# Kernel optimization log

Measured on AMD Instinct MI355X. Metric: run time of the kernel, lower is better.

## Reference

```python
import jax, jax.numpy as jnp
import numpy as np
from jax import lax

DIM = 1024
HEADS = 16
KERNEL = 7
STRIDE = 4
EPS = 1e-5


def setup_inputs() -> dict:
    key = jax.random.key(0)
    ks = jax.random.split(key, 4)
    B, N = 2, 4096
    w_scale = 0.02
    return {
        "x": jax.random.normal(ks[0], (B, N, DIM), dtype=jnp.float32),
        "ln_w": jnp.ones((DIM,), jnp.float32),
        "ln_b": jnp.zeros((DIM,), jnp.float32),
        "Wk": jax.random.normal(ks[1], (DIM, DIM, KERNEL), dtype=jnp.float32) * w_scale,
        "Wv": jax.random.normal(ks[2], (DIM, DIM, KERNEL), dtype=jnp.float32) * w_scale,
        "Wq": jax.random.normal(ks[3], (DIM, DIM, KERNEL), dtype=jnp.float32) * w_scale,
    }


def _conv1d(x_bnd, w):
    # x: (B, N, D) -> conv over sequence dim with 'same' padding; w: (out_ch, in_ch, K)
    x_cn = jnp.transpose(x_bnd, (0, 2, 1))  # (B, D, N)
    pad = KERNEL // 2
    y = lax.conv_general_dilated(
        x_cn, w, window_strides=(1,), padding=[(pad, pad)],
        dimension_numbers=("NCH", "OIH", "NCH"))
    return jnp.transpose(y, (0, 2, 1))  # (B, N, D)


def reference(x, ln_w, ln_b, Wk, Wv, Wq):
    B, N, D = x.shape
    hd = D // HEADS
    # LayerNorm (biased variance, as in torch)
    mu = jnp.mean(x, axis=-1, keepdims=True)
    var = jnp.mean(jnp.square(x - mu), axis=-1, keepdims=True)
    x_n = (x - mu) / jnp.sqrt(var + EPS) * ln_w + ln_b

    K = _conv1d(x_n, Wk)                 # (B, N, D)
    V = _conv1d(x_n, Wv)                 # (B, N, D)
    Q = _conv1d(x_n, Wq)[:, ::STRIDE]    # (B, M, D) windowed queries
    M = Q.shape[1]

    Qh = Q.reshape(B, M, HEADS, hd).transpose(0, 2, 1, 3)  # (B, H, M, hd)
    Kh = K.reshape(B, N, HEADS, hd).transpose(0, 2, 1, 3)  # (B, H, N, hd)
    Vh = V.reshape(B, N, HEADS, hd).transpose(0, 2, 1, 3)  # (B, H, N, hd)

    scale = jnp.sqrt(jnp.asarray(hd, x.dtype))
    scores = jnp.einsum("bhmd,bhnd->bhmn", Qh, Kh) / scale  # (B, H, M, N)
    attn = jax.nn.softmax(scores, axis=-1)
    out = jnp.einsum("bhmn,bhnd->bhmd", attn, Vh)           # (B, H, M, hd)
    out = out.transpose(0, 2, 1, 3).reshape(B, M, D)
    return out + Q
```

## Files before the change

kernel.cpp:

```cpp
#include <hip/hip_runtime.h>

typedef __attribute__((ext_vector_type(4))) float f32x4;
typedef __attribute__((ext_vector_type(16))) float f32x16;
typedef __attribute__((ext_vector_type(8))) short short8;
typedef __attribute__((ext_vector_type(4))) unsigned short u16x4;
typedef __attribute__((ext_vector_type(8))) unsigned short u16x8;

#define AS1 __attribute__((address_space(1)))
#define AS3 __attribute__((address_space(3)))

__device__ __forceinline__ unsigned short f2bf(float f) {
  unsigned u = __float_as_uint(f);
  return (unsigned short)((u + 0x7FFFu + ((u >> 16) & 1u)) >> 16);
}
__device__ __forceinline__ unsigned short f2bf_fast(float f) {
  return (unsigned short)((__float_as_uint(f) + 0x8000u) >> 16);
}

__global__ __launch_bounds__(256) void ln_kernel(
    const float* __restrict__ x, const float* __restrict__ lw,
    const float* __restrict__ lb, unsigned short* __restrict__ xpad) {
  __shared__ float red[8];
  int row = blockIdx.x;
  int b = row >> 12, n = row & 4095;
  const float* xr = x + (size_t)row * 1024;
  int c = threadIdx.x * 4;
  f32x4 v = *(const f32x4*)(xr + c);
  float s = v[0] + v[1] + v[2] + v[3];
  float sq = v[0]*v[0] + v[1]*v[1] + v[2]*v[2] + v[3]*v[3];
#pragma unroll
  for (int off = 32; off; off >>= 1) {
    s  += __shfl_xor(s, off, 64);
    sq += __shfl_xor(sq, off, 64);
  }
  int w = threadIdx.x >> 6;
  if ((threadIdx.x & 63) == 0) { red[w*2] = s; red[w*2+1] = sq; }
  __syncthreads();
  float S  = red[0]+red[2]+red[4]+red[6];
  float SQ = red[1]+red[3]+red[5]+red[7];
  float mean = S * (1.0f/1024.0f);
  float var  = SQ * (1.0f/1024.0f) - mean*mean;
  float rstd = rsqrtf(var + 1e-5f);
  f32x4 wv = *(const f32x4*)(lw + c);
  f32x4 bv = *(const f32x4*)(lb + c);
  u16x4 o;
#pragma unroll
  for (int r = 0; r < 4; ++r) o[r] = f2bf((v[r]-mean)*rstd*wv[r] + bv[r]);
  *(u16x4*)(xpad + (((size_t)(b*4102 + n + 3)) << 10) + c) = o;
}

__global__ __launch_bounds__(256) void repack_kernel(
    const float* __restrict__ Wk, const float* __restrict__ Wv,
    const float* __restrict__ Wq, unsigned short* __restrict__ Wt) {
  __shared__ unsigned short t[7168];
  const float* W = (blockIdx.y == 0) ? Wk : (blockIdx.y == 1) ? Wv : Wq;
  int o = blockIdx.x;
  const float* row = W + (size_t)o * 7168;
  unsigned short* orow = Wt + ((size_t)(blockIdx.y * 1024 + o)) * 7168;
#pragma unroll
  for (int p = 0; p < 7; ++p) {
    int idx = p*1024 + threadIdx.x*4;
    f32x4 v = *(const f32x4*)(row + idx);
#pragma unroll
    for (int e = 0; e < 4; ++e) {
      unsigned j = idx + e;
      unsigned i = (j * 149797u) >> 20;
      unsigned k = j - i*7;
      t[k*1024 + i] = f2bf(v[e]);
    }
  }
  __syncthreads();
#pragma unroll
  for (int p = 0; p < 7; ++p) {
    int idx = p*1024 + threadIdx.x*4;
    *(u16x4*)(orow + idx) = *(const u16x4*)(t + idx);
  }
}

__global__ __launch_bounds__(256, 4) void conv3(
    const unsigned short* __restrict__ Apad,
    const unsigned short* __restrict__ Wt,
    unsigned short* __restrict__ Ksg, unsigned short* __restrict__ Vsg,
    unsigned short* __restrict__ Qsg, float* __restrict__ Qf) {
  __shared__ unsigned short As[128*64];
  __shared__ unsigned short Bs[128*64];
  const int g = blockIdx.x;
  const int tid = threadIdx.x;
  const int w = tid >> 6, l = tid & 63;

  int mode, nt, rt;
  if (g < 1024) {
    int xcol = ((g & 7) << 1) | ((g >> 3) & 1);
    mode = (xcol < 8) ? 0 : 1;
    nt = xcol; rt = g >> 4;
  } else {
    int gq = g - 1024;
    mode = 2; nt = 16 + (gq & 7); rt = gq >> 3;
  }
  const int n0 = nt << 7;
  const int r0 = rt << 7;

  const int lrow = l >> 3;
  const int cs = (l & 7) ^ lrow;
  size_t abase0, astep, bbase0;
  {
    int r = r0 + (w << 5) + lrow;
    int bb, nn;
    if (mode == 2) { bb = r >> 10; nn = (r & 1023) << 2; astep = 8 * 4096; }
    else           { bb = r >> 12; nn = r & 4095;        astep = 8 * 1024; }
    abase0 = (((size_t)(bb*4102 + nn)) << 10) + cs*8;
    int nc = n0 + (w << 5) + lrow;
    bbase0 = (size_t)nc * 7168 + cs*8;
  }

  f32x16 acc[2][2] = {};
  const int wm = (w >> 1) << 6, wn = (w & 1) << 6;
  const int l31 = l & 31, lh = l >> 5, l7 = l & 7;

  for (int k0 = 0; k0 < 7168; k0 += 64) {
    __syncthreads();
#pragma unroll
    for (int t = 0; t < 4; ++t) {
      __builtin_amdgcn_global_load_lds((const AS1 void*)(Apad + abase0 + (size_t)t*astep + k0),
                                       (AS3 void*)(As + (((w << 2) + t) << 9)), 16, 0, 0);
      __builtin_amdgcn_global_load_lds((const AS1 void*)(Wt + bbase0 + (size_t)t*(8*7168) + k0),
                                       (AS3 void*)(Bs + (((w << 2) + t) << 9)), 16, 0, 0);
    }
    __syncthreads();
#pragma unroll
    for (int s2 = 0; s2 < 2; ++s2) {
      short8 af[2][2], bf[2][2];
#pragma unroll
      for (int i = 0; i < 2; ++i)
#pragma unroll
        for (int hs = 0; hs < 2; ++hs) {
          int s = (s2 << 1) | hs;
          int ch = (((s << 1) | lh) ^ l7) << 3;
          af[i][hs] = *(const short8*)(As + (wm + (i<<5) + l31)*64 + ch);
          bf[i][hs] = *(const short8*)(Bs + (wn + (i<<5) + l31)*64 + ch);
        }
#pragma unroll
      for (int hs = 0; hs < 2; ++hs)
#pragma unroll
        for (int i = 0; i < 2; ++i)
#pragma unroll
          for (int j = 0; j < 2; ++j)
            acc[i][j] = __builtin_amdgcn_mfma_f32_32x32x16_bf16(af[i][hs], bf[j][hs], acc[i][j], 0, 0, 0);
    }
  }

  if (mode == 0) {
#pragma unroll
    for (int i = 0; i < 2; ++i) {
      int rgb = r0 + wm + (i<<5);
      int b = rgb >> 12, nbase = rgb & 4095;
#pragma unroll
      for (int j = 0; j < 2; ++j) {
        int cg = n0 + wn + (j<<5) + l31;
        int h = cg >> 6, kd = (cg >> 5) & 1;
        size_t base = ((size_t)(((b*16 + h)*2 + kd)) << 12) * 32 + (size_t)(cg & 31);
#pragma unroll
        for (int r = 0; r < 16; ++r) {
          int nb = nbase + (r & 3) + ((r >> 2) << 3) + (lh << 2);
          Ksg[base + ((size_t)nb << 5)] = f2bf(acc[i][j][r]);
        }
      }
    }
  } else if (mode == 1) {
#pragma unroll
    for (int i = 0; i < 2; ++i) {
      int rgb = r0 + wm + (i<<5);
      int b = rgb >> 12, nbase = rgb & 4095;
      int nc = nbase >> 5;
#pragma unroll
      for (int j = 0; j < 2; ++j) {
        int c = n0 + wn + (j<<5) + l31 - 1024;
        int h = c >> 6, d = c & 63;
        size_t rowbase = ((size_t)((b*16 + h)*128 + nc) * 64 + d) << 5;
#pragma unroll
        for (int g2 = 0; g2 < 4; ++g2) {
          u16x4 pv;
#pragma unroll
          for (int e = 0; e < 4; ++e) pv[e] = f2bf(acc[i][j][g2*4 + e]);
          *(u16x4*)(Vsg + rowbase + (g2 << 3) + (lh << 2)) = pv;
        }
      }
    }
  } else {
#pragma unroll
    for (int i = 0; i < 2; ++i) {
      int rqb = r0 + wm + (i<<5);
#pragma unroll
      for (int j = 0; j < 2; ++j) {
        int cg = (n0 - 2048) + wn + (j<<5) + l31;
        int h = cg >> 6, kd = (cg >> 5) & 1, d32 = cg & 31;
#pragma unroll
        for (int r = 0; r < 16; ++r) {
          int rq = rqb + (r & 3) + ((r >> 2) << 3) + (lh << 2);
          int b = rq >> 10, m = rq & 1023;
          float vv = acc[i][j][r];
          Qsg[(((size_t)((b*16 + h)*2 + kd) * 1024 + m) << 5) + d32] = f2bf(vv);
          Qf[((size_t)rq << 10) + cg] = vv;
        }
      }
    }
  }
}

__global__ __launch_bounds__(256) void attn_kernel(
    const unsigned short* __restrict__ Ksg, const unsigned short* __restrict__ Vsg,
    const unsigned short* __restrict__ Qsg, const float* __restrict__ Qf,
    float* __restrict__ out) {
  __shared__ unsigned short Ks[8192];
  __shared__ unsigned short Vs[8192];
  __shared__ unsigned short Qs[4096];
  __shared__ unsigned short Ps[8704];
  const int tid = threadIdx.x, w = tid >> 6, l = tid & 63;
  const int g = blockIdx.x;
  const int bh = (g & 7) + (((g >> 3) & 3) << 3);
  const int qt = g >> 5;
  const int b = bh >> 4, h = bh & 15;
  const int m0 = qt << 6;
  const int quad = l >> 4, lc = l & 15, l3 = l & 3;
  const float C = 0.18033688011112042f;
  const int lsw = (l & 60) | ((l ^ (l >> 2)) & 3);

  const unsigned short* KgT = Ksg + ((size_t)bh << 18);
  const unsigned short* VgT = Vsg + ((size_t)bh << 18);
  const unsigned short* QgT = Qsg + ((size_t)bh << 16);

#pragma unroll
  for (int p = 0; p < 2; ++p) {
    int t = w*2 + p;
    int kd = t >> 2, ml = (t & 3) << 4;
    __builtin_amdgcn_global_load_lds(
        (const AS1 void*)(QgT + ((size_t)((kd << 10) + m0 + ml) << 5) + lsw*8),
        (AS3 void*)(Qs + (t << 9)), 16, 0, 0);
  }

  float l_run = 0.f;
  f32x4 oacc[4] = {};
  unsigned short* Pw = Ps + w*2176;

  for (int it = 0; it < 32; ++it) {
    int n0 = it << 7;
    __syncthreads();
#pragma unroll
    for (int p = 0; p < 4; ++p) {
      int t = (w << 2) + p;
      __builtin_amdgcn_global_load_lds(
          (const AS1 void*)(KgT + ((size_t)(((t >> 3) << 12) + n0 + ((t & 7) << 4)) << 5) + lsw*8),
          (AS3 void*)(Ks + (t << 9)), 16, 0, 0);
      __builtin_amdgcn_global_load_lds(
          (const AS1 void*)(VgT + ((size_t)((((n0 >> 5) + (t >> 2)) << 6) + ((t & 3) << 4)) << 5) + lsw*8),
          (AS3 void*)(Vs + (t << 9)), 16, 0, 0);
    }
    __syncthreads();

    const int ch = (quad ^ l3) << 3;
    short8 ak[8][2];
#pragma unroll
    for (int k = 0; k < 2; ++k)
#pragma unroll
      for (int ni = 0; ni < 8; ++ni)
        ak[ni][k] = *(const short8*)(Ks + (k << 12) + ((ni<<4) + lc)*32 + ch);

    f32x4 sv[8] = {};
#pragma unroll
    for (int k = 0; k < 2; ++k) {
      short8 bq = *(const short8*)(Qs + (k << 11) + ((w<<4) + lc)*32 + ch);
#pragma unroll
      for (int ni = 0; ni < 8; ++ni)
        sv[ni] = __builtin_amdgcn_mfma_f32_16x16x32_bf16(ak[ni][k], bq, sv[ni], 0, 0, 0);
    }

    float su = 0.f;
#pragma unroll
    for (int ni = 0; ni < 8; ++ni) {
      u16x4 pv;
#pragma unroll
      for (int rr = 0; rr < 4; ++rr) {
        float pp = __builtin_amdgcn_exp2f(sv[ni][rr] * C);
        su += pp;
        pv[rr] = f2bf_fast(pp);
      }
      *(u16x4*)(Pw + lc*136 + (ni<<4) + (quad<<2)) = pv;
    }
    su += __shfl_xor(su, 16, 64);
    su += __shfl_xor(su, 32, 64);
    l_run += su;

#pragma unroll
    for (int kn = 0; kn < 4; ++kn) {
      short8 bp = *(const short8*)(Pw + lc*136 + (kn<<5) + (quad<<3));
#pragma unroll
      for (int dt = 0; dt < 4; ++dt) {
        short8 av = *(const short8*)(Vs + (kn << 11) + ((dt<<4) + lc)*32 + ch);
        oacc[dt] = __builtin_amdgcn_mfma_f32_16x16x32_bf16(av, bp, oacc[dt], 0, 0, 0);
      }
    }
  }

  float invl = 1.0f / l_run;
  int m = m0 + (w<<4) + lc;
#pragma unroll
  for (int dt = 0; dt < 4; ++dt) {
    int d = (dt<<4) + (quad<<2);
    size_t off = (((size_t)(b << 10) + m) << 10) + (h << 6) + d;
    f32x4 qv = *(const f32x4*)(Qf + off);
    f32x4 ov;
#pragma unroll
    for (int rr = 0; rr < 4; ++rr) ov[rr] = oacc[dt][rr]*invl + qv[rr];
    *(f32x4*)(out + off) = ov;
  }
}

extern "C" void kernel_launch(void* const* d_in, const int* in_sizes, int n_in,
                              void* d_out, int out_size, void* d_ws, size_t ws_size,
                              hipStream_t stream) {
  const float* x  = (const float*)d_in[0];
  const float* lw = (const float*)d_in[1];
  const float* lb = (const float*)d_in[2];
  const float* Wk = (const float*)d_in[3];
  const float* Wv = (const float*)d_in[4];
  const float* Wq = (const float*)d_in[5];
  float* out = (float*)d_out;

  char* ws = (char*)d_ws;
  size_t off = 0;
  unsigned short* xpad = (unsigned short*)(ws + off); off += (size_t)2*4102*1024*2;
  unsigned short* Wt   = (unsigned short*)(ws + off); off += (size_t)3072*7168*2;
  unsigned short* Ksg  = (unsigned short*)(ws + off); off += (size_t)32*2*4096*32*2;
  unsigned short* Vsg  = (unsigned short*)(ws + off); off += (size_t)32*128*64*32*2;
  unsigned short* Qsg  = (unsigned short*)(ws + off); off += (size_t)32*2*1024*32*2;
  float*          Qf   = (float*)(ws + off);          off += (size_t)2048*1024*4;

  for (int b = 0; b < 2; ++b) {
    hipMemsetAsync(xpad + (size_t)b*4102*1024, 0, 3*1024*2, stream);
    hipMemsetAsync(xpad + ((size_t)b*4102 + 4099)*1024, 0, 3*1024*2, stream);
  }
  ln_kernel<<<dim3(8192), dim3(256), 0, stream>>>(x, lw, lb, xpad);
  repack_kernel<<<dim3(1024, 3), dim3(256), 0, stream>>>(Wk, Wv, Wq, Wt);
  conv3<<<dim3(1152), dim3(256), 0, stream>>>(xpad, Wt, Ksg, Vsg, Qsg, Qf);
  attn_kernel<<<dim3(512), dim3(256), 0, stream>>>(Ksg, Vsg, Qsg, Qf, out);
}
```

Baseline: 575.0 us.

## Double-buffer LDS tiles in conv3 GEMM to overlap loads with MFMA

Splits the A and B shared-memory tiles of the conv GEMM into two buffers. The next k-slice is now fetched with global_load_lds into the idle buffer while MFMAs consume the current one, which leaves one barrier per iteration instead of two. The cost is double the LDS per block, so launch bounds drop from 4 to 2 blocks per CU. That loses occupancy-based latency hiding in exchange for explicit overlap.

```diff
diff --git a/kernel.cpp b/kernel.cpp
--- a/kernel.cpp
+++ b/kernel.cpp
@@ -77,13 +77,13 @@
   }
 }
 
-__global__ __launch_bounds__(256, 4) void conv3(
+__global__ __launch_bounds__(256, 2) void conv3(
     const unsigned short* __restrict__ Apad,
     const unsigned short* __restrict__ Wt,
     unsigned short* __restrict__ Ksg, unsigned short* __restrict__ Vsg,
     unsigned short* __restrict__ Qsg, float* __restrict__ Qf) {
-  __shared__ unsigned short As[128*64];
-  __shared__ unsigned short Bs[128*64];
+  __shared__ unsigned short As[2][8192];
+  __shared__ unsigned short Bs[2][8192];
   const int g = blockIdx.x;
   const int tid = threadIdx.x;
   const int w = tid >> 6, l = tid & 63;
@@ -116,17 +116,31 @@
   f32x16 acc[2][2] = {};
   const int wm = (w >> 1) << 6, wn = (w & 1) << 6;
   const int l31 = l & 31, lh = l >> 5, l7 = l & 7;
-
-  for (int k0 = 0; k0 < 7168; k0 += 64) {
+  const int wslot = w << 2;
+
+#pragma unroll
+  for (int t = 0; t < 4; ++t) {
+    __builtin_amdgcn_global_load_lds((const AS1 void*)(Apad + abase0 + (size_t)t*astep),
+                                     (AS3 void*)(&As[0][(wslot + t) << 9]), 16, 0, 0);
+    __builtin_amdgcn_global_load_lds((const AS1 void*)(Wt + bbase0 + (size_t)t*(8*7168)),
+                                     (AS3 void*)(&Bs[0][(wslot + t) << 9]), 16, 0, 0);
+  }
+
+  for (int it = 0; it < 112; ++it) {
+    const int cur = it & 1;
     __syncthreads();
-#pragma unroll
-    for (int t = 0; t < 4; ++t) {
-      __builtin_amdgcn_global_load_lds((const AS1 void*)(Apad + abase0 + (size_t)t*astep + k0),
-                                       (AS3 void*)(As + (((w << 2) + t) << 9)), 16, 0, 0);
-      __builtin_amdgcn_global_load_lds((const AS1 void*)(Wt + bbase0 + (size_t)t*(8*7168) + k0),
-                                       (AS3 void*)(Bs + (((w << 2) + t) << 9)), 16, 0, 0);
-    }
-    __syncthreads();
+    if (it + 1 < 112) {
+      const size_t k1 = (size_t)(it + 1) << 6;
+#pragma unroll
+      for (int t = 0; t < 4; ++t) {
+        __builtin_amdgcn_global_load_lds((const AS1 void*)(Apad + abase0 + (size_t)t*astep + k1),
+                                         (AS3 void*)(&As[cur ^ 1][(wslot + t) << 9]), 16, 0, 0);
+        __builtin_amdgcn_global_load_lds((const AS1 void*)(Wt + bbase0 + (size_t)t*(8*7168) + k1),
+                                         (AS3 void*)(&Bs[cur ^ 1][(wslot + t) << 9]), 16, 0, 0);
+      }
+    }
+    const unsigned short* Ac = As[cur];
+    const unsigned short* Bc = Bs[cur];
 #pragma unroll
     for (int s2 = 0; s2 < 2; ++s2) {
       short8 af[2][2], bf[2][2];
@@ -136,8 +150,8 @@
         for (int hs = 0; hs < 2; ++hs) {
           int s = (s2 << 1) | hs;
           int ch = (((s << 1) | lh) ^ l7) << 3;
-          af[i][hs] = *(const short8*)(As + (wm + (i<<5) + l31)*64 + ch);
-          bf[i][hs] = *(const short8*)(Bs + (wn + (i<<5) + l31)*64 + ch);
+          af[i][hs] = *(const short8*)(Ac + (wm + (i<<5) + l31)*64 + ch);
+          bf[i][hs] = *(const short8*)(Bc + (wn + (i<<5) + l31)*64 + ch);
         }
 #pragma unroll
       for (int hs = 0; hs < 2; ++hs)
```

Measured after the change: 696.3 us. 21.1% more time.
